# Optimization experiments

Hardware: AMD Instinct MI355X
Metric: run time of the kernel (lower is better)

## Reference

```python
import jax, jax.numpy as jnp
import numpy as np

NEG_SLOPE = 0.2
EPS = 1e-8

def add_self_loops(edge_index, n_nodes):
    loops = jnp.arange(n_nodes, dtype=edge_index.dtype)
    return jnp.concatenate([edge_index, jnp.stack([loops, loops])], axis=1)

def gatv2_layer(x, edge_index, Wl, Wr, att, bias, concat):
    # x: [N, Fin], edge_index: [2, E] (row0=src j, row1=dst i), att: [H, Fout]
    N = x.shape[0]
    H, Fo = att.shape
    ei = add_self_loops(edge_index, N)
    src, dst = ei[0], ei[1]
    xl = (x @ Wl).reshape(N, H, Fo)
    xr = (x @ Wr).reshape(N, H, Fo)
    s = xl[src] + xr[dst]                                   # [E, H, Fo]
    e = jnp.einsum('ehf,hf->eh', jax.nn.leaky_relu(s, NEG_SLOPE), att)  # [E, H]
    # segment softmax over edges sharing the same destination node
    m = jax.ops.segment_max(e, dst, num_segments=N)          # [N, H]
    ex = jnp.exp(e - m[dst])
    den = jax.ops.segment_sum(ex, dst, num_segments=N)
    alpha = ex / (den[dst] + 1e-16)                          # [E, H]
    out = jax.ops.segment_sum(xl[src] * alpha[:, :, None], dst, num_segments=N)  # [N, H, Fo]
    out = out.reshape(N, H * Fo) if concat else out.mean(axis=1)
    return out + bias

def forward_once(x, edge_index, W1l, W1r, att1, b1, W2l, W2r, att2, b2):
    # eval mode: dropouts are identity
    h = jax.nn.elu(gatv2_layer(x, edge_index, W1l, W1r, att1, b1, concat=True))
    return gatv2_layer(h, edge_index, W2l, W2r, att2, b2, concat=False)

def reference(x1, edge_index1, x2, edge_index2, W1l, W1r, att1, b1, W2l, W2r, att2, b2):
    y = forward_once(x1, edge_index1, W1l, W1r, att1, b1, W2l, W2r, att2, b2)
    z = forward_once(x2, edge_index2, W1l, W1r, att1, b1, W2l, W2r, att2, b2)
    logp_y = jax.nn.log_softmax(y, axis=1)
    logp_z = jax.nn.log_softmax(z, axis=1)
    ny = jnp.maximum(jnp.linalg.norm(y, axis=1), EPS)
    nz = jnp.maximum(jnp.linalg.norm(z, axis=1), EPS)
    cos = jnp.sum(y * z, axis=1) / (ny * nz)
    return (logp_y, 1.0 - cos, logp_z, logp_y, logp_y)

def setup_inputs() -> dict:
    key = jax.random.key(0)
    ks = jax.random.split(key, 12)
    N, E, Fin, HID, H, C = 50000, 800000, 256, 32, 8, 16
    g = lambda k, shape, fan: jax.random.normal(k, shape, jnp.float32) * (1.0 / np.sqrt(fan))
    return {
        'x1': jax.random.normal(ks[0], (N, Fin), jnp.float32),
        'edge_index1': jax.random.randint(ks[1], (2, E), 0, N, jnp.int32),
        'x2': jax.random.normal(ks[2], (N, Fin), jnp.float32),
        'edge_index2': jax.random.randint(ks[3], (2, E), 0, N, jnp.int32),
        'W1l': g(ks[4], (Fin, H * HID), Fin),
        'W1r': g(ks[5], (Fin, H * HID), Fin),
        'att1': g(ks[6], (H, HID), HID),
        'b1': jnp.zeros((H * HID,), jnp.float32),
        'W2l': g(ks[7], (H * HID, 1 * C), H * HID),
        'W2r': g(ks[8], (H * HID, 1 * C), H * HID),
        'att2': g(ks[9], (1, C), C),
        'b2': jnp.zeros((C,), jnp.float32),
    }
```

## Files before the change

kernel.cpp:

```cpp
#include <hip/hip_runtime.h>
#include <hip/hip_bf16.h>
#include <math.h>

#define FIN 256
#define C2  16
#define NEG 0.2f

typedef short bf16x8 __attribute__((ext_vector_type(8)));
typedef float f32x4v __attribute__((ext_vector_type(4)));
typedef float f32x2 __attribute__((ext_vector_type(2)));

__device__ __forceinline__ float bf2f(unsigned short u) {
  union { float f; unsigned int i; } c; c.i = ((unsigned int)u) << 16; return c.f;
}
__device__ __forceinline__ unsigned short f2bf(float f) {
  __hip_bfloat16 b = __float2bfloat16(f);
  return *(unsigned short*)&b;
}
__device__ __forceinline__ f32x2 bfpair(unsigned int u) {
  union { float f; unsigned int i; } lo, hi;
  lo.i = u << 16;
  hi.i = u & 0xffff0000u;
  f32x2 r; r.x = lo.f; r.y = hi.f; return r;
}

__global__ __launch_bounds__(256) void deg_kernel(const int* __restrict__ d1,
    const int* __restrict__ d2, int* __restrict__ deg, int E, int N) {
  int e = blockIdx.x * 256 + threadIdx.x;
  if (e < 2 * E) {
    int g = e >= E;
    int le = g ? e - E : e;
    int d = g ? d2[le] : d1[le];
    atomicAdd(&deg[g * N + d], 1);
  }
}

__global__ __launch_bounds__(1024) void scan_part_kernel(const int* __restrict__ deg,
    int* __restrict__ offs, int* __restrict__ partials, int n) {
  __shared__ int wsum[16], wpref[16];
  int tid = threadIdx.x, lane = tid & 63, wid = tid >> 6;
  int idx = blockIdx.x * 1024 + tid;
  int v = (idx < n) ? deg[idx] : 0;
  int s = v;
#pragma unroll
  for (int o = 1; o < 64; o <<= 1) {
    int t = __shfl_up(s, o, 64);
    if (lane >= o) s += t;
  }
  if (lane == 63) wsum[wid] = s;
  __syncthreads();
  if (tid < 16) {
    int t = wsum[tid];
    int ss = t;
#pragma unroll
    for (int o = 1; o < 16; o <<= 1) {
      int u = __shfl_up(ss, o, 16);
      if (tid >= o) ss += u;
    }
    wpref[tid] = ss - t;
    if (tid == 15) partials[blockIdx.x] = ss;
  }
  __syncthreads();
  if (idx < n) offs[idx] = wpref[wid] + s - v;
}

__global__ __launch_bounds__(1024) void scan_fix_kernel(int* __restrict__ offs,
    const int* __restrict__ partials, int nb, int n) {
  __shared__ int wsum[16], wpref[16];
  __shared__ int carry_s;
  int tid = threadIdx.x, lane = tid & 63, wid = tid >> 6;
  int v = (tid < nb) ? partials[tid] : 0;
  int s = v;
#pragma unroll
  for (int o = 1; o < 64; o <<= 1) {
    int t = __shfl_up(s, o, 64);
    if (lane >= o) s += t;
  }
  if (lane == 63) wsum[wid] = s;
  __syncthreads();
  if (tid < 16) {
    int t = wsum[tid];
    int ss = t;
#pragma unroll
    for (int o = 1; o < 16; o <<= 1) {
      int u = __shfl_up(ss, o, 16);
      if (tid >= o) ss += u;
    }
    wpref[tid] = ss - t;
  }
  __syncthreads();
  s += wpref[wid];
  int b = blockIdx.x;
  if (b == 0) {
    if (tid == nb - 1) offs[n] = s;
  } else if (tid == b - 1) {
    carry_s = s;
  }
  __syncthreads();
  if (b > 0) {
    int idx = b * 1024 + tid;
    if (idx < n) offs[idx] += carry_s;
  }
}

__global__ __launch_bounds__(256) void fill_kernel(const int* __restrict__ ei1,
    const int* __restrict__ ei2, const int* __restrict__ offs,
    int* __restrict__ cnt, int* __restrict__ csr, int E, int N) {
  int e = blockIdx.x * 256 + threadIdx.x;
  if (e < 2 * E) {
    int g = e >= E;
    int le = g ? e - E : e;
    const int* ei = g ? ei2 : ei1;
    int sN = ei[le];
    int d  = ei[le + E];
    int node = g * N + d;
    int pos = offs[node] + atomicAdd(&cnt[node], 1);
    csr[pos] = g * N + sN;
  }
}

__global__ __launch_bounds__(256) void cvt_w_kernel(const float* __restrict__ Wl,
    const float* __restrict__ Wr, unsigned short* __restrict__ Wt) {
  int n = blockIdx.x;
  int k = threadIdx.x;
  float v = (n < 256) ? Wl[k * 256 + n] : Wr[k * 256 + (n - 256)];
  Wt[n * 256 + k] = f2bf(v);
}

__global__ __launch_bounds__(256) void cvt_w2_kernel(const float* __restrict__ Wl,
    const float* __restrict__ Wr, unsigned short* __restrict__ Wt2) {
  int c = blockIdx.x;
  int k = threadIdx.x;
  float v = (c < 16) ? Wl[k * 16 + c] : Wr[k * 16 + (c - 16)];
  Wt2[c * 256 + k] = f2bf(v);
}

#define LDT 72
__global__ __launch_bounds__(512) void gemm_mfma_kernel(
    const float* __restrict__ X1, const float* __restrict__ X2,
    const unsigned short* __restrict__ Bt,
    unsigned short* __restrict__ xlb, unsigned short* __restrict__ xrb,
    int M, int NN) {
  __shared__ __align__(16) unsigned short As[128 * LDT];
  __shared__ __align__(16) unsigned short Bs[128 * LDT];
  int tid = threadIdx.x;
  int G = gridDim.x;
  int q = G >> 3, r = G & 7;
  int b = blockIdx.x;
  int xcd = b & 7, pos = b >> 3;
  int swz = (xcd < r) ? xcd * (q + 1) + pos : r * (q + 1) + (xcd - r) * q + pos;
  int row0 = (swz >> 2) * 128;
  int col0 = (swz & 3) * 128;
  int wid = tid >> 6, lane = tid & 63;
  int wr = wid >> 2, wc = wid & 3;
  int r16 = lane & 15, kb = (lane >> 4) * 8;

  f32x4v acc[4][2];
#pragma unroll
  for (int m = 0; m < 4; m++)
#pragma unroll
    for (int n = 0; n < 2; n++)
#pragma unroll
      for (int qq = 0; qq < 4; qq++) acc[m][n][qq] = 0.f;

  for (int k0 = 0; k0 < 256; k0 += 64) {
#pragma unroll
    for (int it = 0; it < 2; it++) {
      int g = tid + it * 512;
      int rr = g >> 3;
      int ko = (g & 7) * 8;
      int gr = row0 + rr;
      float4 a0 = make_float4(0.f, 0.f, 0.f, 0.f);
      float4 a1 = make_float4(0.f, 0.f, 0.f, 0.f);
      if (gr < M) {
        const float* src = (gr < NN) ? &X1[(size_t)gr * 256]
                                     : &X2[(size_t)(gr - NN) * 256];
        a0 = *(const float4*)&src[k0 + ko];
        a1 = *(const float4*)&src[k0 + ko + 4];
      }
      ushort4 lo, hi;
      lo.x = f2bf(a0.x); lo.y = f2bf(a0.y); lo.z = f2bf(a0.z); lo.w = f2bf(a0.w);
      hi.x = f2bf(a1.x); hi.y = f2bf(a1.y); hi.z = f2bf(a1.z); hi.w = f2bf(a1.w);
      *(ushort4*)&As[rr * LDT + ko] = lo;
      *(ushort4*)&As[rr * LDT + ko + 4] = hi;
      int4 bv = *(const int4*)&Bt[(size_t)(col0 + rr) * 256 + k0 + ko];
      *(int4*)&Bs[rr * LDT + ko] = bv;
    }
    __syncthreads();
#pragma unroll
    for (int kk = 0; kk < 64; kk += 32) {
      bf16x8 af[4], bfr[2];
#pragma unroll
      for (int m = 0; m < 4; m++)
        af[m] = *(const bf16x8*)&As[(wr * 64 + m * 16 + r16) * LDT + kk + kb];
#pragma unroll
      for (int n = 0; n < 2; n++)
        bfr[n] = *(const bf16x8*)&Bs[(wc * 32 + n * 16 + r16) * LDT + kk + kb];
#pragma unroll
      for (int m = 0; m < 4; m++)
#pragma unroll
        for (int n = 0; n < 2; n++)
          acc[m][n] = __builtin_amdgcn_mfma_f32_16x16x32_bf16(af[m], bfr[n], acc[m][n], 0, 0, 0);
    }
    __syncthreads();
  }
  unsigned short* Cb = (col0 < 256) ? xlb : xrb;
  int cbase = (col0 & 255) + wc * 32;
  int rq = (lane >> 4) * 4;
#pragma unroll
  for (int m = 0; m < 4; m++) {
#pragma unroll
    for (int n = 0; n < 2; n++) {
#pragma unroll
      for (int qq = 0; qq < 4; qq++) {
        int gr = row0 + wr * 64 + m * 16 + rq + qq;
        if (gr < M) {
          Cb[(size_t)gr * 256 + cbase + n * 16 + r16] = f2bf(acc[m][n][qq]);
        }
      }
    }
  }
}

#define LDB2 264
__global__ __launch_bounds__(256) void gemm2_mfma_kernel(
    const unsigned short* __restrict__ A, const unsigned short* __restrict__ Bt,
    unsigned short* __restrict__ xl2b, unsigned short* __restrict__ xr2b, int M) {
  __shared__ __align__(16) unsigned short As[256 * LDT];
  __shared__ __align__(16) unsigned short Bs[32 * LDB2];
  int tid = threadIdx.x;
  int row0 = blockIdx.x * 256;
  int wid = tid >> 6, lane = tid & 63;
  int r16 = lane & 15, kb = (lane >> 4) * 8, rq = (lane >> 4) * 4;

#pragma unroll
  for (int it = 0; it < 4; it++) {
    int g = tid + it * 256;
    int rr = g >> 5;
    int ko = (g & 31) * 8;
    *(int4*)&Bs[rr * LDB2 + ko] = *(const int4*)&Bt[rr * 256 + ko];
  }

  f32x4v acc[4][2];
#pragma unroll
  for (int m = 0; m < 4; m++)
#pragma unroll
    for (int n = 0; n < 2; n++)
#pragma unroll
      for (int qq = 0; qq < 4; qq++) acc[m][n][qq] = 0.f;

  for (int k0 = 0; k0 < 256; k0 += 64) {
#pragma unroll
    for (int it = 0; it < 8; it++) {
      int g = tid + it * 256;
      int rr = g >> 3;
      int ko = (g & 7) * 8;
      int gr = row0 + rr;
      int4 av = make_int4(0, 0, 0, 0);
      if (gr < M) av = *(const int4*)&A[(size_t)gr * 256 + k0 + ko];
      *(int4*)&As[rr * LDT + ko] = av;
    }
    __syncthreads();
#pragma unroll
    for (int kk = 0; kk < 64; kk += 32) {
      bf16x8 af[4], bfr[2];
#pragma unroll
      for (int m = 0; m < 4; m++)
        af[m] = *(const bf16x8*)&As[(wid * 64 + m * 16 + r16) * LDT + kk + kb];
#pragma unroll
      for (int n = 0; n < 2; n++)
        bfr[n] = *(const bf16x8*)&Bs[(n * 16 + r16) * LDB2 + k0 + kk + kb];
#pragma unroll
      for (int m = 0; m < 4; m++)
#pragma unroll
        for (int n = 0; n < 2; n++)
          acc[m][n] = __builtin_amdgcn_mfma_f32_16x16x32_bf16(af[m], bfr[n], acc[m][n], 0, 0, 0);
    }
    __syncthreads();
  }
#pragma unroll
  for (int m = 0; m < 4; m++) {
#pragma unroll
    for (int qq = 0; qq < 4; qq++) {
      int gr = row0 + wid * 64 + m * 16 + rq + qq;
      if (gr < M) {
        xl2b[(size_t)gr * 16 + r16] = f2bf(acc[m][0][qq]);
        xr2b[(size_t)gr * 16 + r16] = f2bf(acc[m][1][qq]);
      }
    }
  }
}

__global__ __launch_bounds__(256) void gat1_kernel(const unsigned short* __restrict__ xlb,
    unsigned short* xrb, const float* __restrict__ att, const float* __restrict__ bias,
    const int* __restrict__ offs, const int* __restrict__ csr, int M) {
  int w = threadIdx.x >> 6, lane = threadIdx.x & 63;
  int i = blockIdx.x * 4 + w;
  if (i >= M) return;
  i = __builtin_amdgcn_readfirstlane(i);
  const uint2* rows = (const uint2*)xlb;
  uint2 ul = rows[(size_t)i * 64 + lane];
  uint2 ur = ((const uint2*)(xrb + (size_t)i * 256))[lane];
  f32x2 xl01 = bfpair(ul.x), xl23 = bfpair(ul.y);
  f32x2 xr01 = bfpair(ur.x), xr23 = bfpair(ur.y);
  float4 a4 = ((const float4*)att)[lane];
  f32x2 a01; a01.x = a4.x; a01.y = a4.y;
  f32x2 a23; a23.x = a4.z; a23.y = a4.w;

  f32x2 t01 = xl01 + xr01, t23 = xl23 + xr23;
  f32x2 l01 = __builtin_elementwise_max(t01, t01 * NEG);
  f32x2 l23 = __builtin_elementwise_max(t23, t23 * NEG);
  f32x2 ps = l01 * a01 + l23 * a23;
  float p = ps.x + ps.y;
  p += __shfl_xor(p, 1, 8);
  p += __shfl_xor(p, 2, 8);
  p += __shfl_xor(p, 4, 8);
  float m = p, ssum = 1.f;
  f32x2 O01 = xl01, O23 = xl23;

  int e = offs[i], end = offs[i + 1];
  int rem = end - e;

  int ja0 = __builtin_amdgcn_readfirstlane(rem > 0 ? csr[e + 0] : i);
  int ja1 = __builtin_amdgcn_readfirstlane(rem > 1 ? csr[e + 1] : i);
  uint2 ua0 = rows[(size_t)ja0 * 64 + lane];
  uint2 ua1 = rows[(size_t)ja1 * 64 + lane];
  int jb0 = __builtin_amdgcn_readfirstlane(rem > 2 ? csr[e + 2] : i);
  int jb1 = __builtin_amdgcn_readfirstlane(rem > 3 ? csr[e + 3] : i);
  uint2 ub0 = rows[(size_t)jb0 * 64 + lane];
  uint2 ub1 = rows[(size_t)jb1 * 64 + lane];
  int jc0 = __builtin_amdgcn_readfirstlane(rem > 4 ? csr[e + 4] : i);
  int jc1 = __builtin_amdgcn_readfirstlane(rem > 5 ? csr[e + 5] : i);
  uint2 uc0 = rows[(size_t)jc0 * 64 + lane];
  uint2 uc1 = rows[(size_t)jc1 * 64 + lane];

  while (rem >= 2) {
    int jn0 = __builtin_amdgcn_readfirstlane(rem > 6 ? csr[e + 6] : i);
    int jn1 = __builtin_amdgcn_readfirstlane(rem > 7 ? csr[e + 7] : i);
    uint2 un0 = rows[(size_t)jn0 * 64 + lane];
    uint2 un1 = rows[(size_t)jn1 * 64 + lane];
    f32x2 x001 = bfpair(ua0.x), x023 = bfpair(ua0.y);
    f32x2 x101 = bfpair(ua1.x), x123 = bfpair(ua1.y);
    f32x2 q01 = x001 + xr01, q23 = x023 + xr23;
    f32x2 r01 = x101 + xr01, r23 = x123 + xr23;
    f32x2 g01 = __builtin_elementwise_max(q01, q01 * NEG);
    f32x2 g23 = __builtin_elementwise_max(q23, q23 * NEG);
    f32x2 k01 = __builtin_elementwise_max(r01, r01 * NEG);
    f32x2 k23 = __builtin_elementwise_max(r23, r23 * NEG);
    f32x2 s0v = g01 * a01 + g23 * a23;
    f32x2 s1v = k01 * a01 + k23 * a23;
    float p0 = s0v.x + s0v.y;
    float p1 = s1v.x + s1v.y;
    p0 += __shfl_xor(p0, 1, 8);
    p1 += __shfl_xor(p1, 1, 8);
    p0 += __shfl_xor(p0, 2, 8);
    p1 += __shfl_xor(p1, 2, 8);
    p0 += __shfl_xor(p0, 4, 8);
    p1 += __shfl_xor(p1, 4, 8);
    float mx = fmaxf(p0, p1);
    if (!__all(mx <= m + 8.f)) {
      float mn = fmaxf(m, mx);
      float sc = __expf(m - mn);
      O01 *= sc; O23 *= sc; ssum *= sc; m = mn;
    }
    float w0 = __expf(p0 - m), w1 = __expf(p1 - m);
    O01 += w0 * x001 + w1 * x101;
    O23 += w0 * x023 + w1 * x123;
    ssum += w0 + w1;
    ua0 = ub0; ua1 = ub1;
    ub0 = uc0; ub1 = uc1;
    uc0 = un0; uc1 = un1;
    e += 2; rem -= 2;
  }
  if (rem == 1) {
    f32x2 x001 = bfpair(ua0.x), x023 = bfpair(ua0.y);
    f32x2 q01 = x001 + xr01, q23 = x023 + xr23;
    f32x2 g01 = __builtin_elementwise_max(q01, q01 * NEG);
    f32x2 g23 = __builtin_elementwise_max(q23, q23 * NEG);
    f32x2 s0v = g01 * a01 + g23 * a23;
    float p0 = s0v.x + s0v.y;
    p0 += __shfl_xor(p0, 1, 8);
    p0 += __shfl_xor(p0, 2, 8);
    p0 += __shfl_xor(p0, 4, 8);
    if (!__all(p0 <= m + 8.f)) {
      float mn = fmaxf(m, p0);
      float sc = __expf(m - mn);
      O01 *= sc; O23 *= sc; ssum *= sc; m = mn;
    }
    float w0 = __expf(p0 - m);
    O01 += w0 * x001;
    O23 += w0 * x023;
    ssum += w0;
  }
  float inv = 1.f / (ssum + 1e-16f);
  float4 b4 = ((const float4*)bias)[lane];
  float h0 = O01.x * inv + b4.x;
  float h1 = O01.y * inv + b4.y;
  float h2 = O23.x * inv + b4.z;
  float h3 = O23.y * inv + b4.w;
  h0 = h0 > 0.f ? h0 : (__expf(h0) - 1.f);
  h1 = h1 > 0.f ? h1 : (__expf(h1) - 1.f);
  h2 = h2 > 0.f ? h2 : (__expf(h2) - 1.f);
  h3 = h3 > 0.f ? h3 : (__expf(h3) - 1.f);
  ushort4 o;
  o.x = f2bf(h0); o.y = f2bf(h1); o.z = f2bf(h2); o.w = f2bf(h3);
  ((ushort4*)(xrb + (size_t)i * 256))[lane] = o;
}

__global__ __launch_bounds__(256) void gat2_kernel(const unsigned short* __restrict__ xl2b,
    const unsigned short* __restrict__ xr2b, const float* __restrict__ att,
    const float* __restrict__ b2, const int* __restrict__ offs,
    const int* __restrict__ csr, float* __restrict__ y2, int M) {
  int grp = threadIdx.x >> 4, c = threadIdx.x & 15;
  int i = blockIdx.x * 16 + grp;
  if (i >= M) return;
  float xli = bf2f(xl2b[(size_t)i * 16 + c]);
  float xri = bf2f(xr2b[(size_t)i * 16 + c]);
  float a = att[c];
  float v = xli + xri; v = fmaxf(v, NEG * v);
  float p = v * a;
#pragma unroll
  for (int o = 8; o >= 1; o >>= 1) p += __shfl_xor(p, o, 16);
  float m = p, ssum = 1.0f, O = xli;

  int e = offs[i], end = offs[i + 1];
  int rem = end - e;

  int ja0 = rem > 0 ? csr[e + 0] : i;
  int ja1 = rem > 1 ? csr[e + 1] : i;
  float xa0 = bf2f(xl2b[(size_t)ja0 * 16 + c]);
  float xa1 = bf2f(xl2b[(size_t)ja1 * 16 + c]);
  int jb0 = rem > 2 ? csr[e + 2] : i;
  int jb1 = rem > 3 ? csr[e + 3] : i;
  float xb0 = bf2f(xl2b[(size_t)jb0 * 16 + c]);
  float xb1 = bf2f(xl2b[(size_t)jb1 * 16 + c]);
  int jc0 = rem > 4 ? csr[e + 4] : i;
  int jc1 = rem > 5 ? csr[e + 5] : i;
  float xc0 = bf2f(xl2b[(size_t)jc0 * 16 + c]);
  float xc1 = bf2f(xl2b[(size_t)jc1 * 16 + c]);

  while (rem >= 2) {
    int jn0 = rem > 6 ? csr[e + 6] : i;
    int jn1 = rem > 7 ? csr[e + 7] : i;
    float xn0 = bf2f(xl2b[(size_t)jn0 * 16 + c]);
    float xn1 = bf2f(xl2b[(size_t)jn1 * 16 + c]);
    float q0 = xa0 + xri; q0 = fmaxf(q0, NEG * q0);
    float q1 = xa1 + xri; q1 = fmaxf(q1, NEG * q1);
    float p0 = q0 * a, p1 = q1 * a;
#pragma unroll
    for (int o = 8; o >= 1; o >>= 1) {
      p0 += __shfl_xor(p0, o, 16);
      p1 += __shfl_xor(p1, o, 16);
    }
    float mx = fmaxf(p0, p1);
    if (!__all(mx <= m + 8.f)) {
      float mn = fmaxf(m, mx);
      float sc = __expf(m - mn);
      O *= sc; ssum *= sc; m = mn;
    }
    float w0 = __expf(p0 - m), w1 = __expf(p1 - m);
    O += w0 * xa0 + w1 * xa1;
    ssum += w0 + w1;
    xa0 = xb0; xa1 = xb1;
    xb0 = xc0; xb1 = xc1;
    xc0 = xn0; xc1 = xn1;
    e += 2; rem -= 2;
  }
  if (rem == 1) {
    float q0 = xa0 + xri; q0 = fmaxf(q0, NEG * q0);
    float p0 = q0 * a;
#pragma unroll
    for (int o = 8; o >= 1; o >>= 1) p0 += __shfl_xor(p0, o, 16);
    if (!__all(p0 <= m + 8.f)) {
      float mn = fmaxf(m, p0);
      float sc = __expf(m - mn);
      O *= sc; ssum *= sc; m = mn;
    }
    float w0 = __expf(p0 - m);
    O += w0 * xa0;
    ssum += w0;
  }
  y2[(size_t)i * C2 + c] = O / (ssum + 1e-16f) + b2[c];
}

__global__ __launch_bounds__(256) void finalize_kernel(const float* __restrict__ y,
    const float* __restrict__ z, float* __restrict__ out, int N) {
  int grp = threadIdx.x >> 4, c = threadIdx.x & 15;
  int i = blockIdx.x * 16 + grp;
  if (i >= N) return;
  float yv = y[(size_t)i * C2 + c];
  float zv = z[(size_t)i * C2 + c];
  float my = yv;
#pragma unroll
  for (int o = 8; o >= 1; o >>= 1) my = fmaxf(my, __shfl_xor(my, o, 16));
  float sy = __expf(yv - my);
#pragma unroll
  for (int o = 8; o >= 1; o >>= 1) sy += __shfl_xor(sy, o, 16);
  float lpy = yv - my - __logf(sy);
  float mz = zv;
#pragma unroll
  for (int o = 8; o >= 1; o >>= 1) mz = fmaxf(mz, __shfl_xor(mz, o, 16));
  float sz = __expf(zv - mz);
#pragma unroll
  for (int o = 8; o >= 1; o >>= 1) sz += __shfl_xor(sz, o, 16);
  float lpz = zv - mz - __logf(sz);
  float dot = yv * zv, ny2 = yv * yv, nz2 = zv * zv;
#pragma unroll
  for (int o = 8; o >= 1; o >>= 1) {
    dot += __shfl_xor(dot, o, 16);
    ny2 += __shfl_xor(ny2, o, 16);
    nz2 += __shfl_xor(nz2, o, 16);
  }
  float ny = fmaxf(sqrtf(ny2), 1e-8f);
  float nz = fmaxf(sqrtf(nz2), 1e-8f);
  float cosv = dot / (ny * nz);
  size_t o1 = (size_t)N * C2;
  size_t o2 = o1 + N;
  size_t o3 = o2 + (size_t)N * C2;
  size_t o4 = o3 + (size_t)N * C2;
  size_t idx = (size_t)i * C2 + c;
  out[idx] = lpy;
  if (c == 0) out[o1 + i] = 1.0f - cosv;
  out[o2 + idx] = lpz;
  out[o3 + idx] = lpy;
  out[o4 + idx] = lpy;
}

extern "C" void kernel_launch(void* const* d_in, const int* in_sizes, int n_in,
                              void* d_out, int out_size, void* d_ws, size_t ws_size,
                              hipStream_t stream) {
  const float* x1   = (const float*)d_in[0];
  const int*   ei1  = (const int*)d_in[1];
  const float* x2   = (const float*)d_in[2];
  const int*   ei2  = (const int*)d_in[3];
  const float* W1l  = (const float*)d_in[4];
  const float* W1r  = (const float*)d_in[5];
  const float* att1 = (const float*)d_in[6];
  const float* b1   = (const float*)d_in[7];
  const float* W2l  = (const float*)d_in[8];
  const float* W2r  = (const float*)d_in[9];
  const float* att2 = (const float*)d_in[10];
  const float* b2   = (const float*)d_in[11];
  const int N = in_sizes[0] / FIN;
  const int E = in_sizes[1] / 2;
  const int M = 2 * N;
  float* out = (float*)d_out;

  char* w = (char*)d_ws;
  size_t off = 0;
  auto carve = [&](size_t bytes) -> void* {
    void* p = w + off;
    off += (bytes + 255) & ~(size_t)255;
    return p;
  };
  unsigned short* xlb  = (unsigned short*)carve((size_t)M * 256 * 2);
  unsigned short* xrb  = (unsigned short*)carve((size_t)M * 256 * 2);
  unsigned short* Wt   = (unsigned short*)carve(512 * 256 * 2);
  unsigned short* Wt2  = (unsigned short*)carve(32 * 256 * 2);
  unsigned short* xl2b = (unsigned short*)carve((size_t)M * 16 * 2);
  unsigned short* xr2b = (unsigned short*)carve((size_t)M * 16 * 2);
  float* y2  = (float*)carve((size_t)M * 16 * 4);
  int* deg  = (int*)carve((size_t)M * 4);
  int* cnt  = (int*)carve((size_t)M * 4);
  int* offs = (int*)carve((size_t)(M + 1) * 4);
  int* csr  = (int*)carve((size_t)2 * E * 4);
  int* partials = (int*)carve(128 * 4);
  (void)ws_size; (void)n_in; (void)out_size;

  const size_t zero_bytes = (size_t)((char*)cnt - (char*)deg) + (size_t)M * 4;
  hipMemsetAsync(deg, 0, zero_bytes, stream);

  const int NB = (M + 1023) / 1024;

  cvt_w_kernel<<<512, 256, 0, stream>>>(W1l, W1r, Wt);
  cvt_w2_kernel<<<32, 256, 0, stream>>>(W2l, W2r, Wt2);

  deg_kernel<<<(2 * E + 255) / 256, 256, 0, stream>>>(ei1 + E, ei2 + E, deg, E, N);
  scan_part_kernel<<<NB, 1024, 0, stream>>>(deg, offs, partials, M);
  scan_fix_kernel<<<NB, 1024, 0, stream>>>(offs, partials, NB, M);
  fill_kernel<<<(2 * E + 255) / 256, 256, 0, stream>>>(ei1, ei2, offs, cnt, csr, E, N);

  int RB = (M + 127) / 128;
  gemm_mfma_kernel<<<RB * 4, 512, 0, stream>>>(x1, x2, Wt, xlb, xrb, M, N);
  gat1_kernel<<<(M + 3) / 4, 256, 0, stream>>>(xlb, xrb, att1, b1, offs, csr, M);
  gemm2_mfma_kernel<<<(M + 255) / 256, 256, 0, stream>>>(xrb, Wt2, xl2b, xr2b, M);
  gat2_kernel<<<(M + 15) / 16, 256, 0, stream>>>(xl2b, xr2b, att2, b2, offs, csr, y2, M);

  finalize_kernel<<<(N + 15) / 16, 256, 0, stream>>>(y2, y2 + (size_t)N * 16, out, N);
}
```

Before: 408.8 us.

## Unroll GAT edge loops by four, use exp2, vectorize CSR build, merge weight conversion

The two GAT aggregation kernels now process four neighbours per iteration with a two-stage prefetch instead of two, masking tail edges with a large negative score rather than running a separate remainder path. Attention weights are pre-scaled by log2(e) so that exp2f replaces __expf. The degree and fill kernels each read four edges per thread with int4 loads, and the two weight-conversion kernels are merged into one launch. The intent is more memory-level parallelism in the gathers and fewer launches, at the cost of extra register pressure and some wasted work on padded tail edges.

```diff
diff --git a/kernel.cpp b/kernel.cpp
--- a/kernel.cpp
+++ b/kernel.cpp
@@ -5,6 +5,7 @@
 #define FIN 256
 #define C2  16
 #define NEG 0.2f
+#define LOG2E 1.4426950408889634f
 
 typedef short bf16x8 __attribute__((ext_vector_type(8)));
 typedef float f32x4v __attribute__((ext_vector_type(4)));
@@ -24,14 +25,25 @@
   f32x2 r; r.x = lo.f; r.y = hi.f; return r;
 }
 
-__global__ __launch_bounds__(256) void deg_kernel(const int* __restrict__ d1,
-    const int* __restrict__ d2, int* __restrict__ deg, int E, int N) {
-  int e = blockIdx.x * 256 + threadIdx.x;
-  if (e < 2 * E) {
-    int g = e >= E;
-    int le = g ? e - E : e;
-    int d = g ? d2[le] : d1[le];
-    atomicAdd(&deg[g * N + d], 1);
+__global__ __launch_bounds__(256) void deg_kernel(const int* __restrict__ ei1,
+    const int* __restrict__ ei2, int* __restrict__ deg, int E, int N) {
+  int EQ = (E + 3) >> 2;
+  int q = blockIdx.x * 256 + threadIdx.x;
+  if (q >= 2 * EQ) return;
+  int g = q >= EQ;
+  int lq = g ? q - EQ : q;
+  const int* dstp = (g ? ei2 : ei1) + E;
+  int base = g * N;
+  int e0 = lq * 4;
+  if (e0 + 3 < E) {
+    int4 d4 = *(const int4*)&dstp[e0];
+    atomicAdd(&deg[base + d4.x], 1);
+    atomicAdd(&deg[base + d4.y], 1);
+    atomicAdd(&deg[base + d4.z], 1);
+    atomicAdd(&deg[base + d4.w], 1);
+  } else {
+    for (int k = 0; k < 4 && e0 + k < E; k++)
+      atomicAdd(&deg[base + dstp[e0 + k]], 1);
   }
 }
 
@@ -106,33 +118,44 @@
 __global__ __launch_bounds__(256) void fill_kernel(const int* __restrict__ ei1,
     const int* __restrict__ ei2, const int* __restrict__ offs,
     int* __restrict__ cnt, int* __restrict__ csr, int E, int N) {
-  int e = blockIdx.x * 256 + threadIdx.x;
-  if (e < 2 * E) {
-    int g = e >= E;
-    int le = g ? e - E : e;
-    const int* ei = g ? ei2 : ei1;
-    int sN = ei[le];
-    int d  = ei[le + E];
-    int node = g * N + d;
-    int pos = offs[node] + atomicAdd(&cnt[node], 1);
-    csr[pos] = g * N + sN;
-  }
-}
-
-__global__ __launch_bounds__(256) void cvt_w_kernel(const float* __restrict__ Wl,
-    const float* __restrict__ Wr, unsigned short* __restrict__ Wt) {
+  int EQ = (E + 3) >> 2;
+  int q = blockIdx.x * 256 + threadIdx.x;
+  if (q >= 2 * EQ) return;
+  int g = q >= EQ;
+  int lq = g ? q - EQ : q;
+  const int* ei = g ? ei2 : ei1;
+  int base = g * N;
+  int e0 = lq * 4;
+  if (e0 + 3 < E) {
+    int4 s4 = *(const int4*)&ei[e0];
+    int4 d4 = *(const int4*)&ei[E + e0];
+    int n0 = base + d4.x, n1 = base + d4.y, n2 = base + d4.z, n3 = base + d4.w;
+    csr[offs[n0] + atomicAdd(&cnt[n0], 1)] = base + s4.x;
+    csr[offs[n1] + atomicAdd(&cnt[n1], 1)] = base + s4.y;
+    csr[offs[n2] + atomicAdd(&cnt[n2], 1)] = base + s4.z;
+    csr[offs[n3] + atomicAdd(&cnt[n3], 1)] = base + s4.w;
+  } else {
+    for (int k = 0; k < 4 && e0 + k < E; k++) {
+      int node = base + ei[E + e0 + k];
+      csr[offs[node] + atomicAdd(&cnt[node], 1)] = base + ei[e0 + k];
+    }
+  }
+}
+
+__global__ __launch_bounds__(256) void cvt_w_kernel(const float* __restrict__ W1l,
+    const float* __restrict__ W1r, const float* __restrict__ W2l,
+    const float* __restrict__ W2r, unsigned short* __restrict__ Wt,
+    unsigned short* __restrict__ Wt2) {
   int n = blockIdx.x;
   int k = threadIdx.x;
-  float v = (n < 256) ? Wl[k * 256 + n] : Wr[k * 256 + (n - 256)];
-  Wt[n * 256 + k] = f2bf(v);
-}
-
-__global__ __launch_bounds__(256) void cvt_w2_kernel(const float* __restrict__ Wl,
-    const float* __restrict__ Wr, unsigned short* __restrict__ Wt2) {
-  int c = blockIdx.x;
-  int k = threadIdx.x;
-  float v = (c < 16) ? Wl[k * 16 + c] : Wr[k * 16 + (c - 16)];
-  Wt2[c * 256 + k] = f2bf(v);
+  if (n < 512) {
+    float v = (n < 256) ? W1l[k * 256 + n] : W1r[k * 256 + (n - 256)];
+    Wt[n * 256 + k] = f2bf(v);
+  } else {
+    int c = n - 512;
+    float v = (c < 16) ? W2l[k * 16 + c] : W2r[k * 16 + (c - 16)];
+    Wt2[c * 256 + k] = f2bf(v);
+  }
 }
 
 #define LDT 72
@@ -304,8 +327,8 @@
   f32x2 xl01 = bfpair(ul.x), xl23 = bfpair(ul.y);
   f32x2 xr01 = bfpair(ur.x), xr23 = bfpair(ur.y);
   float4 a4 = ((const float4*)att)[lane];
-  f32x2 a01; a01.x = a4.x; a01.y = a4.y;
-  f32x2 a23; a23.x = a4.z; a23.y = a4.w;
+  f32x2 a01; a01.x = a4.x * LOG2E; a01.y = a4.y * LOG2E;
+  f32x2 a23; a23.x = a4.z * LOG2E; a23.y = a4.w * LOG2E;
 
   f32x2 t01 = xl01 + xr01, t23 = xl23 + xr23;
   f32x2 l01 = __builtin_elementwise_max(t01, t01 * NEG);
@@ -318,80 +341,97 @@
   float m = p, ssum = 1.f;
   f32x2 O01 = xl01, O23 = xl23;
 
-  int e = offs[i], end = offs[i + 1];
-  int rem = end - e;
-
-  int ja0 = __builtin_amdgcn_readfirstlane(rem > 0 ? csr[e + 0] : i);
-  int ja1 = __builtin_amdgcn_readfirstlane(rem > 1 ? csr[e + 1] : i);
-  uint2 ua0 = rows[(size_t)ja0 * 64 + lane];
-  uint2 ua1 = rows[(size_t)ja1 * 64 + lane];
-  int jb0 = __builtin_amdgcn_readfirstlane(rem > 2 ? csr[e + 2] : i);
-  int jb1 = __builtin_amdgcn_readfirstlane(rem > 3 ? csr[e + 3] : i);
-  uint2 ub0 = rows[(size_t)jb0 * 64 + lane];
-  uint2 ub1 = rows[(size_t)jb1 * 64 + lane];
-  int jc0 = __builtin_amdgcn_readfirstlane(rem > 4 ? csr[e + 4] : i);
-  int jc1 = __builtin_amdgcn_readfirstlane(rem > 5 ? csr[e + 5] : i);
-  uint2 uc0 = rows[(size_t)jc0 * 64 + lane];
-  uint2 uc1 = rows[(size_t)jc1 * 64 + lane];
-
-  while (rem >= 2) {
-    int jn0 = __builtin_amdgcn_readfirstlane(rem > 6 ? csr[e + 6] : i);
-    int jn1 = __builtin_amdgcn_readfirstlane(rem > 7 ? csr[e + 7] : i);
-    uint2 un0 = rows[(size_t)jn0 * 64 + lane];
-    uint2 un1 = rows[(size_t)jn1 * 64 + lane];
-    f32x2 x001 = bfpair(ua0.x), x023 = bfpair(ua0.y);
-    f32x2 x101 = bfpair(ua1.x), x123 = bfpair(ua1.y);
-    f32x2 q01 = x001 + xr01, q23 = x023 + xr23;
-    f32x2 r01 = x101 + xr01, r23 = x123 + xr23;
-    f32x2 g01 = __builtin_elementwise_max(q01, q01 * NEG);
-    f32x2 g23 = __builtin_elementwise_max(q23, q23 * NEG);
-    f32x2 k01 = __builtin_elementwise_max(r01, r01 * NEG);
-    f32x2 k23 = __builtin_elementwise_max(r23, r23 * NEG);
-    f32x2 s0v = g01 * a01 + g23 * a23;
-    f32x2 s1v = k01 * a01 + k23 * a23;
-    float p0 = s0v.x + s0v.y;
-    float p1 = s1v.x + s1v.y;
+  int e0 = offs[i], end = offs[i + 1];
+  int rem = end - e0;
+  int iters = (rem + 3) >> 2;
+
+  uint2 ua0, ua1, ua2, ua3, ub0, ub1, ub2, ub3;
+  {
+    int idx0 = e0 + 0, idx1 = e0 + 1, idx2 = e0 + 2, idx3 = e0 + 3;
+    int j0 = __builtin_amdgcn_readfirstlane(idx0 < end ? csr[idx0] : i);
+    int j1 = __builtin_amdgcn_readfirstlane(idx1 < end ? csr[idx1] : i);
+    int j2 = __builtin_amdgcn_readfirstlane(idx2 < end ? csr[idx2] : i);
+    int j3 = __builtin_amdgcn_readfirstlane(idx3 < end ? csr[idx3] : i);
+    ua0 = rows[(size_t)j0 * 64 + lane];
+    ua1 = rows[(size_t)j1 * 64 + lane];
+    ua2 = rows[(size_t)j2 * 64 + lane];
+    ua3 = rows[(size_t)j3 * 64 + lane];
+    idx0 += 4; idx1 += 4; idx2 += 4; idx3 += 4;
+    j0 = __builtin_amdgcn_readfirstlane(idx0 < end ? csr[idx0] : i);
+    j1 = __builtin_amdgcn_readfirstlane(idx1 < end ? csr[idx1] : i);
+    j2 = __builtin_amdgcn_readfirstlane(idx2 < end ? csr[idx2] : i);
+    j3 = __builtin_amdgcn_readfirstlane(idx3 < end ? csr[idx3] : i);
+    ub0 = rows[(size_t)j0 * 64 + lane];
+    ub1 = rows[(size_t)j1 * 64 + lane];
+    ub2 = rows[(size_t)j2 * 64 + lane];
+    ub3 = rows[(size_t)j3 * 64 + lane];
+  }
+
+  for (int t = 0; t < iters; t++) {
+    int nb = e0 + (t + 2) * 4;
+    int j0 = __builtin_amdgcn_readfirstlane(nb + 0 < end ? csr[nb + 0] : i);
+    int j1 = __builtin_amdgcn_readfirstlane(nb + 1 < end ? csr[nb + 1] : i);
+    int j2 = __builtin_amdgcn_readfirstlane(nb + 2 < end ? csr[nb + 2] : i);
+    int j3 = __builtin_amdgcn_readfirstlane(nb + 3 < end ? csr[nb + 3] : i);
+    uint2 un0 = rows[(size_t)j0 * 64 + lane];
+    uint2 un1 = rows[(size_t)j1 * 64 + lane];
+    uint2 un2 = rows[(size_t)j2 * 64 + lane];
+    uint2 un3 = rows[(size_t)j3 * 64 + lane];
+
+    f32x2 x0a = bfpair(ua0.x), x0b = bfpair(ua0.y);
+    f32x2 x1a = bfpair(ua1.x), x1b = bfpair(ua1.y);
+    f32x2 x2a = bfpair(ua2.x), x2b = bfpair(ua2.y);
+    f32x2 x3a = bfpair(ua3.x), x3b = bfpair(ua3.y);
+    f32x2 q0a = x0a + xr01, q0b = x0b + xr23;
+    f32x2 q1a = x1a + xr01, q1b = x1b + xr23;
+    f32x2 q2a = x2a + xr01, q2b = x2b + xr23;
+    f32x2 q3a = x3a + xr01, q3b = x3b + xr23;
+    q0a = __builtin_elementwise_max(q0a, q0a * NEG);
+    q0b = __builtin_elementwise_max(q0b, q0b * NEG);
+    q1a = __builtin_elementwise_max(q1a, q1a * NEG);
+    q1b = __builtin_elementwise_max(q1b, q1b * NEG);
+    q2a = __builtin_elementwise_max(q2a, q2a * NEG);
+    q2b = __builtin_elementwise_max(q2b, q2b * NEG);
+    q3a = __builtin_elementwise_max(q3a, q3a * NEG);
+    q3b = __builtin_elementwise_max(q3b, q3b * NEG);
+    f32x2 s0 = q0a * a01 + q0b * a23;
+    f32x2 s1 = q1a * a01 + q1b * a23;
+    f32x2 s2 = q2a * a01 + q2b * a23;
+    f32x2 s3 = q3a * a01 + q3b * a23;
+    float p0 = s0.x + s0.y, p1 = s1.x + s1.y, p2 = s2.x + s2.y, p3 = s3.x + s3.y;
     p0 += __shfl_xor(p0, 1, 8);
     p1 += __shfl_xor(p1, 1, 8);
+    p2 += __shfl_xor(p2, 1, 8);
+    p3 += __shfl_xor(p3, 1, 8);
     p0 += __shfl_xor(p0, 2, 8);
     p1 += __shfl_xor(p1, 2, 8);
+    p2 += __shfl_xor(p2, 2, 8);
+    p3 += __shfl_xor(p3, 2, 8);
     p0 += __shfl_xor(p0, 4, 8);
     p1 += __shfl_xor(p1, 4, 8);
-    float mx = fmaxf(p0, p1);
+    p2 += __shfl_xor(p2, 4, 8);
+    p3 += __shfl_xor(p3, 4, 8);
+    int base = e0 + t * 4;
+    if (base + 1 >= end) p1 = -3.0e38f;
+    if (base + 2 >= end) p2 = -3.0e38f;
+    if (base + 3 >= end) p3 = -3.0e38f;
+    float mx = fmaxf(fmaxf(p0, p1), fmaxf(p2, p3));
     if (!__all(mx <= m + 8.f)) {
       float mn = fmaxf(m, mx);
-      float sc = __expf(m - mn);
+      float sc = exp2f(m - mn);
       O01 *= sc; O23 *= sc; ssum *= sc; m = mn;
     }
-    float w0 = __expf(p0 - m), w1 = __expf(p1 - m);
-    O01 += w0 * x001 + w1 * x101;
-    O23 += w0 * x023 + w1 * x123;
-    ssum += w0 + w1;
-    ua0 = ub0; ua1 = ub1;
-    ub0 = uc0; ub1 = uc1;
-    uc0 = un0; uc1 = un1;
-    e += 2; rem -= 2;
-  }
-  if (rem == 1) {
-    f32x2 x001 = bfpair(ua0.x), x023 = bfpair(ua0.y);
-    f32x2 q01 = x001 + xr01, q23 = x023 + xr23;
-    f32x2 g01 = __builtin_elementwise_max(q01, q01 * NEG);
-    f32x2 g23 = __builtin_elementwise_max(q23, q23 * NEG);
-    f32x2 s0v = g01 * a01 + g23 * a23;
-    float p0 = s0v.x + s0v.y;
-    p0 += __shfl_xor(p0, 1, 8);
-    p0 += __shfl_xor(p0, 2, 8);
-    p0 += __shfl_xor(p0, 4, 8);
-    if (!__all(p0 <= m + 8.f)) {
-      float mn = fmaxf(m, p0);
-      float sc = __expf(m - mn);
-      O01 *= sc; O23 *= sc; ssum *= sc; m = mn;
-    }
-    float w0 = __expf(p0 - m);
-    O01 += w0 * x001;
-    O23 += w0 * x023;
-    ssum += w0;
-  }
+    float w0 = exp2f(p0 - m), w1 = exp2f(p1 - m);
+    float w2 = exp2f(p2 - m), w3 = exp2f(p3 - m);
+    O01 += w0 * x0a + w1 * x1a;
+    O23 += w0 * x0b + w1 * x1b;
+    O01 += w2 * x2a + w3 * x3a;
+    O23 += w2 * x2b + w3 * x3b;
+    ssum += (w0 + w1) + (w2 + w3);
+    ua0 = ub0; ua1 = ub1; ua2 = ub2; ua3 = ub3;
+    ub0 = un0; ub1 = un1; ub2 = un2; ub3 = un3;
+  }
+
   float inv = 1.f / (ssum + 1e-16f);
   float4 b4 = ((const float4*)bias)[lane];
   float h0 = O01.x * inv + b4.x;
@@ -416,69 +456,76 @@
   if (i >= M) return;
   float xli = bf2f(xl2b[(size_t)i * 16 + c]);
   float xri = bf2f(xr2b[(size_t)i * 16 + c]);
-  float a = att[c];
+  float a = att[c] * LOG2E;
   float v = xli + xri; v = fmaxf(v, NEG * v);
   float p = v * a;
 #pragma unroll
   for (int o = 8; o >= 1; o >>= 1) p += __shfl_xor(p, o, 16);
   float m = p, ssum = 1.0f, O = xli;
 
-  int e = offs[i], end = offs[i + 1];
-  int rem = end - e;
-
-  int ja0 = rem > 0 ? csr[e + 0] : i;
-  int ja1 = rem > 1 ? csr[e + 1] : i;
-  float xa0 = bf2f(xl2b[(size_t)ja0 * 16 + c]);
-  float xa1 = bf2f(xl2b[(size_t)ja1 * 16 + c]);
-  int jb0 = rem > 2 ? csr[e + 2] : i;
-  int jb1 = rem > 3 ? csr[e + 3] : i;
-  float xb0 = bf2f(xl2b[(size_t)jb0 * 16 + c]);
-  float xb1 = bf2f(xl2b[(size_t)jb1 * 16 + c]);
-  int jc0 = rem > 4 ? csr[e + 4] : i;
-  int jc1 = rem > 5 ? csr[e + 5] : i;
-  float xc0 = bf2f(xl2b[(size_t)jc0 * 16 + c]);
-  float xc1 = bf2f(xl2b[(size_t)jc1 * 16 + c]);
-
-  while (rem >= 2) {
-    int jn0 = rem > 6 ? csr[e + 6] : i;
-    int jn1 = rem > 7 ? csr[e + 7] : i;
-    float xn0 = bf2f(xl2b[(size_t)jn0 * 16 + c]);
-    float xn1 = bf2f(xl2b[(size_t)jn1 * 16 + c]);
+  int e0 = offs[i], end = offs[i + 1];
+  int rem = end - e0;
+  int iters = (rem + 3) >> 2;
+
+  float xa0, xa1, xa2, xa3, xb0, xb1, xb2, xb3;
+  {
+    int j0 = (e0 + 0 < end) ? csr[e0 + 0] : i;
+    int j1 = (e0 + 1 < end) ? csr[e0 + 1] : i;
+    int j2 = (e0 + 2 < end) ? csr[e0 + 2] : i;
+    int j3 = (e0 + 3 < end) ? csr[e0 + 3] : i;
+    xa0 = bf2f(xl2b[(size_t)j0 * 16 + c]);
+    xa1 = bf2f(xl2b[(size_t)j1 * 16 + c]);
+    xa2 = bf2f(xl2b[(size_t)j2 * 16 + c]);
+    xa3 = bf2f(xl2b[(size_t)j3 * 16 + c]);
+    j0 = (e0 + 4 < end) ? csr[e0 + 4] : i;
+    j1 = (e0 + 5 < end) ? csr[e0 + 5] : i;
+    j2 = (e0 + 6 < end) ? csr[e0 + 6] : i;
+    j3 = (e0 + 7 < end) ? csr[e0 + 7] : i;
+    xb0 = bf2f(xl2b[(size_t)j0 * 16 + c]);
+    xb1 = bf2f(xl2b[(size_t)j1 * 16 + c]);
+    xb2 = bf2f(xl2b[(size_t)j2 * 16 + c]);
+    xb3 = bf2f(xl2b[(size_t)j3 * 16 + c]);
+  }
+
+  for (int t = 0; t < iters; t++) {
+    int nb = e0 + (t + 2) * 4;
+    int j0 = (nb + 0 < end) ? csr[nb + 0] : i;
+    int j1 = (nb + 1 < end) ? csr[nb + 1] : i;
+    int j2 = (nb + 2 < end) ? csr[nb + 2] : i;
+    int j3 = (nb + 3 < end) ? csr[nb + 3] : i;
+    float xn0 = bf2f(xl2b[(size_t)j0 * 16 + c]);
+    float xn1 = bf2f(xl2b[(size_t)j1 * 16 + c]);
+    float xn2 = bf2f(xl2b[(size_t)j2 * 16 + c]);
+    float xn3 = bf2f(xl2b[(size_t)j3 * 16 + c]);
+
     float q0 = xa0 + xri; q0 = fmaxf(q0, NEG * q0);
     float q1 = xa1 + xri; q1 = fmaxf(q1, NEG * q1);
-    float p0 = q0 * a, p1 = q1 * a;
+    float q2 = xa2 + xri; q2 = fmaxf(q2, NEG * q2);
+    float q3 = xa3 + xri; q3 = fmaxf(q3, NEG * q3);
+    float p0 = q0 * a, p1 = q1 * a, p2 = q2 * a, p3 = q3 * a;
 #pragma unroll
     for (int o = 8; o >= 1; o >>= 1) {
       p0 += __shfl_xor(p0, o, 16);
       p1 += __shfl_xor(p1, o, 16);
-    }
-    float mx = fmaxf(p0, p1);
+      p2 += __shfl_xor(p2, o, 16);
+      p3 += __shfl_xor(p3, o, 16);
+    }
+    int base = e0 + t * 4;
+    if (base + 1 >= end) p1 = -3.0e38f;
+    if (base + 2 >= end) p2 = -3.0e38f;
+    if (base + 3 >= end) p3 = -3.0e38f;
+    float mx = fmaxf(fmaxf(p0, p1), fmaxf(p2, p3));
     if (!__all(mx <= m + 8.f)) {
       float mn = fmaxf(m, mx);
-      float sc = __expf(m - mn);
+      float sc = exp2f(m - mn);
       O *= sc; ssum *= sc; m = mn;
     }
-    float w0 = __expf(p0 - m), w1 = __expf(p1 - m);
-    O += w0 * xa0 + w1 * xa1;
-    ssum += w0 + w1;
-    xa0 = xb0; xa1 = xb1;
-    xb0 = xc0; xb1 = xc1;
-    xc0 = xn0; xc1 = xn1;
-    e += 2; rem -= 2;
-  }
-  if (rem == 1) {
-    float q0 = xa0 + xri; q0 = fmaxf(q0, NEG * q0);
-    float p0 = q0 * a;
-#pragma unroll
-    for (int o = 8; o >= 1; o >>= 1) p0 += __shfl_xor(p0, o, 16);
-    if (!__all(p0 <= m + 8.f)) {
-      float mn = fmaxf(m, p0);
-      float sc = __expf(m - mn);
-      O *= sc; ssum *= sc; m = mn;
-    }
-    float w0 = __expf(p0 - m);
-    O += w0 * xa0;
-    ssum += w0;
+    float w0 = exp2f(p0 - m), w1 = exp2f(p1 - m);
+    float w2 = exp2f(p2 - m), w3 = exp2f(p3 - m);
+    O += w0 * xa0 + w1 * xa1 + w2 * xa2 + w3 * xa3;
+    ssum += (w0 + w1) + (w2 + w3);
+    xa0 = xb0; xa1 = xb1; xa2 = xb2; xa3 = xb3;
+    xb0 = xn0; xb1 = xn1; xb2 = xn2; xb3 = xn3;
   }
   y2[(size_t)i * C2 + c] = O / (ssum + 1e-16f) + b2[c];
 }
@@ -571,14 +618,14 @@
   hipMemsetAsync(deg, 0, zero_bytes, stream);
 
   const int NB = (M + 1023) / 1024;
-
-  cvt_w_kernel<<<512, 256, 0, stream>>>(W1l, W1r, Wt);
-  cvt_w2_kernel<<<32, 256, 0, stream>>>(W2l, W2r, Wt2);
-
-  deg_kernel<<<(2 * E + 255) / 256, 256, 0, stream>>>(ei1 + E, ei2 + E, deg, E, N);
+  const int EQ = (E + 3) >> 2;
+
+  cvt_w_kernel<<<544, 256, 0, stream>>>(W1l, W1r, W2l, W2r, Wt, Wt2);
+
+  deg_kernel<<<(2 * EQ + 255) / 256, 256, 0, stream>>>(ei1, ei2, deg, E, N);
   scan_part_kernel<<<NB, 1024, 0, stream>>>(deg, offs, partials, M);
   scan_fix_kernel<<<NB, 1024, 0, stream>>>(offs, partials, NB, M);
-  fill_kernel<<<(2 * E + 255) / 256, 256, 0, stream>>>(ei1, ei2, offs, cnt, csr, E, N);
+  fill_kernel<<<(2 * EQ + 255) / 256, 256, 0, stream>>>(ei1, ei2, offs, cnt, csr, E, N);
 
   int RB = (M + 127) / 128;
   gemm_mfma_kernel<<<RB * 4, 512, 0, stream>>>(x1, x2, Wt, xlb, xrb, M, N);
```

After: 422.1 us. +3.3%, slower.

## Vectorize CSR build kernels, merge weight conversions, use exp2 with prescaled attention

Applied to the files above, without the earlier changes.

The degree and fill kernels now handle four edges per thread using int4 loads, and the two weight-conversion kernels are merged into one launch. The attention vectors are prescaled by log2(e) so the softmax can call exp2f instead of __expf. The point is to cut launch count and per-edge index load overhead. Issuing four atomics per thread may raise contention or lower parallelism in the CSR build.

```diff
diff --git a/kernel.cpp b/kernel.cpp
--- a/kernel.cpp
+++ b/kernel.cpp
@@ -5,6 +5,7 @@
 #define FIN 256
 #define C2  16
 #define NEG 0.2f
+#define LOG2E 1.4426950408889634f
 
 typedef short bf16x8 __attribute__((ext_vector_type(8)));
 typedef float f32x4v __attribute__((ext_vector_type(4)));
@@ -24,14 +25,25 @@
   f32x2 r; r.x = lo.f; r.y = hi.f; return r;
 }
 
-__global__ __launch_bounds__(256) void deg_kernel(const int* __restrict__ d1,
-    const int* __restrict__ d2, int* __restrict__ deg, int E, int N) {
-  int e = blockIdx.x * 256 + threadIdx.x;
-  if (e < 2 * E) {
-    int g = e >= E;
-    int le = g ? e - E : e;
-    int d = g ? d2[le] : d1[le];
-    atomicAdd(&deg[g * N + d], 1);
+__global__ __launch_bounds__(256) void deg_kernel(const int* __restrict__ ei1,
+    const int* __restrict__ ei2, int* __restrict__ deg, int E, int N) {
+  int EQ = (E + 3) >> 2;
+  int q = blockIdx.x * 256 + threadIdx.x;
+  if (q >= 2 * EQ) return;
+  int g = q >= EQ;
+  int lq = g ? q - EQ : q;
+  const int* dstp = (g ? ei2 : ei1) + E;
+  int base = g * N;
+  int e0 = lq * 4;
+  if (e0 + 3 < E) {
+    int4 d4 = *(const int4*)&dstp[e0];
+    atomicAdd(&deg[base + d4.x], 1);
+    atomicAdd(&deg[base + d4.y], 1);
+    atomicAdd(&deg[base + d4.z], 1);
+    atomicAdd(&deg[base + d4.w], 1);
+  } else {
+    for (int k = 0; k < 4 && e0 + k < E; k++)
+      atomicAdd(&deg[base + dstp[e0 + k]], 1);
   }
 }
 
@@ -106,33 +118,44 @@
 __global__ __launch_bounds__(256) void fill_kernel(const int* __restrict__ ei1,
     const int* __restrict__ ei2, const int* __restrict__ offs,
     int* __restrict__ cnt, int* __restrict__ csr, int E, int N) {
-  int e = blockIdx.x * 256 + threadIdx.x;
-  if (e < 2 * E) {
-    int g = e >= E;
-    int le = g ? e - E : e;
-    const int* ei = g ? ei2 : ei1;
-    int sN = ei[le];
-    int d  = ei[le + E];
-    int node = g * N + d;
-    int pos = offs[node] + atomicAdd(&cnt[node], 1);
-    csr[pos] = g * N + sN;
-  }
-}
-
-__global__ __launch_bounds__(256) void cvt_w_kernel(const float* __restrict__ Wl,
-    const float* __restrict__ Wr, unsigned short* __restrict__ Wt) {
+  int EQ = (E + 3) >> 2;
+  int q = blockIdx.x * 256 + threadIdx.x;
+  if (q >= 2 * EQ) return;
+  int g = q >= EQ;
+  int lq = g ? q - EQ : q;
+  const int* ei = g ? ei2 : ei1;
+  int base = g * N;
+  int e0 = lq * 4;
+  if (e0 + 3 < E) {
+    int4 s4 = *(const int4*)&ei[e0];
+    int4 d4 = *(const int4*)&ei[E + e0];
+    int n0 = base + d4.x, n1 = base + d4.y, n2 = base + d4.z, n3 = base + d4.w;
+    csr[offs[n0] + atomicAdd(&cnt[n0], 1)] = base + s4.x;
+    csr[offs[n1] + atomicAdd(&cnt[n1], 1)] = base + s4.y;
+    csr[offs[n2] + atomicAdd(&cnt[n2], 1)] = base + s4.z;
+    csr[offs[n3] + atomicAdd(&cnt[n3], 1)] = base + s4.w;
+  } else {
+    for (int k = 0; k < 4 && e0 + k < E; k++) {
+      int node = base + ei[E + e0 + k];
+      csr[offs[node] + atomicAdd(&cnt[node], 1)] = base + ei[e0 + k];
+    }
+  }
+}
+
+__global__ __launch_bounds__(256) void cvt_w_kernel(const float* __restrict__ W1l,
+    const float* __restrict__ W1r, const float* __restrict__ W2l,
+    const float* __restrict__ W2r, unsigned short* __restrict__ Wt,
+    unsigned short* __restrict__ Wt2) {
   int n = blockIdx.x;
   int k = threadIdx.x;
-  float v = (n < 256) ? Wl[k * 256 + n] : Wr[k * 256 + (n - 256)];
-  Wt[n * 256 + k] = f2bf(v);
-}
-
-__global__ __launch_bounds__(256) void cvt_w2_kernel(const float* __restrict__ Wl,
-    const float* __restrict__ Wr, unsigned short* __restrict__ Wt2) {
-  int c = blockIdx.x;
-  int k = threadIdx.x;
-  float v = (c < 16) ? Wl[k * 16 + c] : Wr[k * 16 + (c - 16)];
-  Wt2[c * 256 + k] = f2bf(v);
+  if (n < 512) {
+    float v = (n < 256) ? W1l[k * 256 + n] : W1r[k * 256 + (n - 256)];
+    Wt[n * 256 + k] = f2bf(v);
+  } else {
+    int c = n - 512;
+    float v = (c < 16) ? W2l[k * 16 + c] : W2r[k * 16 + (c - 16)];
+    Wt2[c * 256 + k] = f2bf(v);
+  }
 }
 
 #define LDT 72
@@ -304,8 +327,8 @@
   f32x2 xl01 = bfpair(ul.x), xl23 = bfpair(ul.y);
   f32x2 xr01 = bfpair(ur.x), xr23 = bfpair(ur.y);
   float4 a4 = ((const float4*)att)[lane];
-  f32x2 a01; a01.x = a4.x; a01.y = a4.y;
-  f32x2 a23; a23.x = a4.z; a23.y = a4.w;
+  f32x2 a01; a01.x = a4.x * LOG2E; a01.y = a4.y * LOG2E;
+  f32x2 a23; a23.x = a4.z * LOG2E; a23.y = a4.w * LOG2E;
 
   f32x2 t01 = xl01 + xr01, t23 = xl23 + xr23;
   f32x2 l01 = __builtin_elementwise_max(t01, t01 * NEG);
@@ -360,10 +383,10 @@
     float mx = fmaxf(p0, p1);
     if (!__all(mx <= m + 8.f)) {
       float mn = fmaxf(m, mx);
-      float sc = __expf(m - mn);
+      float sc = exp2f(m - mn);
       O01 *= sc; O23 *= sc; ssum *= sc; m = mn;
     }
-    float w0 = __expf(p0 - m), w1 = __expf(p1 - m);
+    float w0 = exp2f(p0 - m), w1 = exp2f(p1 - m);
     O01 += w0 * x001 + w1 * x101;
     O23 += w0 * x023 + w1 * x123;
     ssum += w0 + w1;
@@ -384,10 +407,10 @@
     p0 += __shfl_xor(p0, 4, 8);
     if (!__all(p0 <= m + 8.f)) {
       float mn = fmaxf(m, p0);
-      float sc = __expf(m - mn);
+      float sc = exp2f(m - mn);
       O01 *= sc; O23 *= sc; ssum *= sc; m = mn;
     }
-    float w0 = __expf(p0 - m);
+    float w0 = exp2f(p0 - m);
     O01 += w0 * x001;
     O23 += w0 * x023;
     ssum += w0;
@@ -416,7 +439,7 @@
   if (i >= M) return;
   float xli = bf2f(xl2b[(size_t)i * 16 + c]);
   float xri = bf2f(xr2b[(size_t)i * 16 + c]);
-  float a = att[c];
+  float a = att[c] * LOG2E;
   float v = xli + xri; v = fmaxf(v, NEG * v);
   float p = v * a;
 #pragma unroll
@@ -455,10 +478,10 @@
     float mx = fmaxf(p0, p1);
     if (!__all(mx <= m + 8.f)) {
       float mn = fmaxf(m, mx);
-      float sc = __expf(m - mn);
+      float sc = exp2f(m - mn);
       O *= sc; ssum *= sc; m = mn;
     }
-    float w0 = __expf(p0 - m), w1 = __expf(p1 - m);
+    float w0 = exp2f(p0 - m), w1 = exp2f(p1 - m);
     O += w0 * xa0 + w1 * xa1;
     ssum += w0 + w1;
     xa0 = xb0; xa1 = xb1;
@@ -473,10 +496,10 @@
     for (int o = 8; o >= 1; o >>= 1) p0 += __shfl_xor(p0, o, 16);
     if (!__all(p0 <= m + 8.f)) {
       float mn = fmaxf(m, p0);
-      float sc = __expf(m - mn);
+      float sc = exp2f(m - mn);
       O *= sc; ssum *= sc; m = mn;
     }
-    float w0 = __expf(p0 - m);
+    float w0 = exp2f(p0 - m);
     O += w0 * xa0;
     ssum += w0;
   }
@@ -571,14 +594,14 @@
   hipMemsetAsync(deg, 0, zero_bytes, stream);
 
   const int NB = (M + 1023) / 1024;
-
-  cvt_w_kernel<<<512, 256, 0, stream>>>(W1l, W1r, Wt);
-  cvt_w2_kernel<<<32, 256, 0, stream>>>(W2l, W2r, Wt2);
-
-  deg_kernel<<<(2 * E + 255) / 256, 256, 0, stream>>>(ei1 + E, ei2 + E, deg, E, N);
+  const int EQ = (E + 3) >> 2;
+
+  cvt_w_kernel<<<544, 256, 0, stream>>>(W1l, W1r, W2l, W2r, Wt, Wt2);
+
+  deg_kernel<<<(2 * EQ + 255) / 256, 256, 0, stream>>>(ei1, ei2, deg, E, N);
   scan_part_kernel<<<NB, 1024, 0, stream>>>(deg, offs, partials, M);
   scan_fix_kernel<<<NB, 1024, 0, stream>>>(offs, partials, NB, M);
-  fill_kernel<<<(2 * E + 255) / 256, 256, 0, stream>>>(ei1, ei2, offs, cnt, csr, E, N);
+  fill_kernel<<<(2 * EQ + 255) / 256, 256, 0, stream>>>(ei1, ei2, offs, cnt, csr, E, N);
 
   int RB = (M + 127) / 128;
   gemm_mfma_kernel<<<RB * 4, 512, 0, stream>>>(x1, x2, Wt, xlb, xrb, M, N);
```

Result: no change. 410.9 us (+0.5%).
